# Optimization experiments

Hardware: AMD Instinct MI355X
Metric: run time of the kernel (lower is better)

## Reference

```python
import jax, jax.numpy as jnp
import numpy as np

NUM_ENTITIES = 100000
NUM_RELATIONS = 500
DIM = 256
NUM_TRIANGLES = 300000
NUM_TETRAS = 150000
ET_EDGES = 900000   # ~3 entities per triangle
TT_EDGES = 600000   # ~4 triangles per tetra
ENT_TET_EDGES = 600000
BATCH = 8192


def _mean_aggregate(src_idx, dst_idx, src, num_dst):
    """Scatter-mean of src[src_idx] into num_dst buckets keyed by dst_idx."""
    agg = jax.ops.segment_sum(src[src_idx], dst_idx, num_segments=num_dst)
    cnt = jax.ops.segment_sum(jnp.ones_like(dst_idx, dtype=src.dtype), dst_idx,
                              num_segments=num_dst)
    return agg / jnp.maximum(cnt, 1.0)[:, None]


def setup_inputs() -> dict:
    key = jax.random.key(0)
    ks = jax.random.split(key, 16)
    s = 1.0 / np.sqrt(DIM)
    E = jax.random.normal(ks[0], (NUM_ENTITIES, DIM), jnp.float32) * s
    R = jax.random.normal(ks[1], (NUM_RELATIONS, DIM), jnp.float32) * s
    lin2_w = jax.random.normal(ks[2], (DIM, DIM), jnp.float32) * s
    lin2_b = jnp.zeros((DIM,), jnp.float32)
    lin3_w = jax.random.normal(ks[3], (DIM, DIM), jnp.float32) * s
    lin3_b = jnp.zeros((DIM,), jnp.float32)
    t2e_w = jax.random.normal(ks[4], (DIM, DIM), jnp.float32) * s
    t2e_b = jnp.zeros((DIM,), jnp.float32)
    fusion_alpha = jnp.zeros((2,), jnp.float32)
    gamma = jnp.array([12.0], jnp.float32)
    # bipartite edge lists: row 0 = src indices, row 1 = dst indices
    et = jnp.stack([
        jax.random.randint(ks[5], (ET_EDGES,), 0, NUM_ENTITIES),
        jax.random.randint(ks[6], (ET_EDGES,), 0, NUM_TRIANGLES)], axis=0)
    tt = jnp.stack([
        jax.random.randint(ks[7], (TT_EDGES,), 0, NUM_TRIANGLES),
        jax.random.randint(ks[8], (TT_EDGES,), 0, NUM_TETRAS)], axis=0)
    # entity_tetra_index: row 0 = entity, row 1 = tetra (flipped inside model)
    etet = jnp.stack([
        jax.random.randint(ks[9], (ENT_TET_EDGES,), 0, NUM_ENTITIES),
        jax.random.randint(ks[10], (ENT_TET_EDGES,), 0, NUM_TETRAS)], axis=0)
    triples = jnp.stack([
        jax.random.randint(ks[11], (BATCH,), 0, NUM_ENTITIES),
        jax.random.randint(ks[12], (BATCH,), 0, NUM_RELATIONS),
        jax.random.randint(ks[13], (BATCH,), 0, NUM_ENTITIES)], axis=1)
    return {"E": E, "R": R, "lin2_w": lin2_w, "lin2_b": lin2_b,
            "lin3_w": lin3_w, "lin3_b": lin3_b, "t2e_w": t2e_w, "t2e_b": t2e_b,
            "fusion_alpha": fusion_alpha, "gamma": gamma,
            "entity_triangle_index": et, "triangle_tetra_index": tt,
            "entity_tetra_index": etet, "triples": triples,
            "num_triangles": NUM_TRIANGLES, "num_tetras": NUM_TETRAS}


def reference(E, R, lin2_w, lin2_b, lin3_w, lin3_b, t2e_w, t2e_b,
              fusion_alpha, gamma, entity_triangle_index, triangle_tetra_index,
              entity_tetra_index, triples, num_triangles, num_tetras):
    # gnn2: entity -> triangle (scatter-mean + Linear + ReLU)
    tri_agg = _mean_aggregate(entity_triangle_index[0], entity_triangle_index[1],
                              E, num_triangles)                      # [T, d]
    tri_emb = jax.nn.relu(tri_agg @ lin2_w.T + lin2_b)
    # gnn3: triangle -> tetra
    tet_agg = _mean_aggregate(triangle_tetra_index[0], triangle_tetra_index[1],
                              tri_emb, num_tetras)                   # [K, d]
    tet_emb = jax.nn.relu(tet_agg @ lin3_w.T + lin3_b)
    tet_proj = tet_emb @ t2e_w.T + t2e_b                             # [K, d]
    # tetra -> entity (edge index flipped: src=tetra, dst=entity)
    v_topo = _mean_aggregate(entity_tetra_index[1], entity_tetra_index[0],
                             tet_proj, E.shape[0])                   # [N, d]
    # learned fusion
    w = jax.nn.softmax(fusion_alpha)
    V = w[0] * E + w[1] * v_topo
    # TransE scoring: gamma - ||V[h] + R[r] - V[t]||
    h, r, t = triples[:, 0], triples[:, 1], triples[:, 2]
    diff = V[h] + R[r] - V[t]
    return gamma[0] - jnp.sqrt(jnp.sum(diff * diff, axis=-1))
```

## Files before the change

### kernel.cpp

```cpp
#include <hip/hip_runtime.h>
#include <hip/hip_bf16.h>
#include <math.h>

#define DIM 256
#define SBS 256
#define SIT 16
#define NT   300000
#define NTET 150000

typedef __attribute__((ext_vector_type(8))) short          bf16x8;
typedef __attribute__((ext_vector_type(8))) unsigned short u16x8;
typedef __attribute__((ext_vector_type(4))) float          f32x4;

__device__ inline float b2f(unsigned short u) {
    union { unsigned int i; float f; } c; c.i = ((unsigned int)u) << 16; return c.f;
}
__device__ inline unsigned short f2b(float f) {
    __hip_bfloat16 h = __float2bfloat16(f);
    return *reinterpret_cast<unsigned short*>(&h);
}
__device__ inline short f2bs(float f) { return (short)f2b(f); }
__device__ inline bool bmget(const unsigned* bm, int i) {
    return (bm[i >> 5] >> (i & 31)) & 1u;
}
__device__ inline void gll16(const void* g, void* l) {
    __builtin_amdgcn_global_load_lds(
        (const __attribute__((address_space(1))) unsigned int*)g,
        (__attribute__((address_space(3))) unsigned int*)l, 16, 0, 0);
}

__global__ __launch_bounds__(256) void k_cast3(
    const float* __restrict__ w2, const float* __restrict__ w3,
    const float* __restrict__ wt, unsigned short* __restrict__ out)
{
    int i = (blockIdx.x * 256 + threadIdx.x) * 4;
    const float* src; int l;
    if (i < 65536)       { src = w2; l = i; }
    else if (i < 131072) { src = w3; l = i - 65536; }
    else                 { src = wt; l = i - 131072; }
    float4 v = *(const float4*)(src + l);
    ushort4 o; o.x = f2b(v.x); o.y = f2b(v.y); o.z = f2b(v.z); o.w = f2b(v.w);
    *(ushort4*)(out + i) = o;
}

__global__ __launch_bounds__(256) void k_mark(
    const int* __restrict__ trip, unsigned* __restrict__ bm, int B)
{
    int i = blockIdx.x * 256 + threadIdx.x;
    if (i < 2 * B) {
        int ent = trip[(i >> 1) * 3 + ((i & 1) ? 2 : 0)];
        atomicOr(&bm[ent >> 5], 1u << (ent & 31));
    }
}

__global__ __launch_bounds__(256) void k_markf(
    const int* __restrict__ mi, const int* __restrict__ ci,
    const unsigned* __restrict__ bmIn, unsigned* __restrict__ bmOut, int n)
{
    int e = blockIdx.x * 256 + threadIdx.x;
    if (e < n && bmget(bmIn, ci[e])) {
        int m = mi[e];
        unsigned msk = 1u << (m & 31);
        if (!(bmOut[m >> 5] & msk)) atomicOr(&bmOut[m >> 5], msk);
    }
}

__global__ __launch_bounds__(256) void k_bits(
    const unsigned* __restrict__ bm, int* __restrict__ out, int n)
{
    int i = blockIdx.x * 256 + threadIdx.x;
    if (i < n) out[i] = (bm[i >> 5] >> (i & 31)) & 1u;
}

__global__ __launch_bounds__(256) void k_count_all(
    const int* __restrict__ et, const int* __restrict__ tt, const int* __restrict__ etet,
    const unsigned* __restrict__ bmTri, const unsigned* __restrict__ bmTet,
    const unsigned* __restrict__ bmEnt, int* __restrict__ cnt,
    int ET, int TT, int ETET)
{
    int e = blockIdx.x * 256 + threadIdx.x;
    if (e < ET) {
        int d = et[ET + e];
        if (bmget(bmTri, d)) atomicAdd(&cnt[d], 1);
    } else if (e < ET + TT) {
        int i = e - ET;
        int d = tt[TT + i];
        if (bmget(bmTet, d)) atomicAdd(&cnt[NT + d], 1);
    } else if (e < ET + TT + ETET) {
        int i = e - ET - TT;
        int d = etet[i];
        if (bmget(bmEnt, d)) atomicAdd(&cnt[NT + NTET + d], 1);
    }
}

__global__ __launch_bounds__(SBS) void k_scan_block(
    const int* __restrict__ cnt, int* __restrict__ rowOff,
    int* __restrict__ blockSums, int n)
{
    __shared__ int lds[SBS];
    const int t = threadIdx.x;
    const int tbase = blockIdx.x * SBS * SIT + t * SIT;
    int v[SIT]; int tsum = 0;
    #pragma unroll
    for (int i = 0; i < SIT; ++i) {
        int idx = tbase + i;
        v[i] = (idx < n) ? cnt[idx] : 0;
        tsum += v[i];
    }
    lds[t] = tsum;
    __syncthreads();
    #pragma unroll
    for (int off = 1; off < SBS; off <<= 1) {
        int y = (t >= off) ? lds[t - off] : 0;
        __syncthreads();
        lds[t] += y;
        __syncthreads();
    }
    int incl = lds[t];
    int run = incl - tsum;
    #pragma unroll
    for (int i = 0; i < SIT; ++i) {
        int idx = tbase + i;
        if (idx < n) rowOff[idx] = run;
        run += v[i];
    }
    if (t == SBS - 1) blockSums[blockIdx.x] = incl;
}

__global__ __launch_bounds__(SBS) void k_scan_sums(int* __restrict__ bs, int nb)
{
    __shared__ int lds[SBS];
    const int t = threadIdx.x;
    int v = (t < nb) ? bs[t] : 0;
    lds[t] = v;
    __syncthreads();
    #pragma unroll
    for (int off = 1; off < SBS; off <<= 1) {
        int y = (t >= off) ? lds[t - off] : 0;
        __syncthreads();
        lds[t] += y;
        __syncthreads();
    }
    if (t < nb) {
        bs[t] = lds[t] - v;
        if (t == nb - 1) bs[nb] = lds[t];
    }
}

__global__ __launch_bounds__(256) void k_scan_add(
    int* __restrict__ rowOff, int* __restrict__ cursor,
    const int* __restrict__ bs, int n, int nb, int ncur)
{
    int i = blockIdx.x * 256 + threadIdx.x;
    if (i < n) {
        int v = rowOff[i] + bs[i / (SBS * SIT)];
        rowOff[i] = v;
        if (i < ncur) cursor[i] = v;
    }
    if (i == 0) rowOff[n] = bs[nb];
}

__global__ __launch_bounds__(256) void k_place_all(
    const int* __restrict__ et, const int* __restrict__ tt, const int* __restrict__ etet,
    const unsigned* __restrict__ bmTri, const unsigned* __restrict__ bmTet,
    const unsigned* __restrict__ bmEnt, int* __restrict__ cursor,
    int* __restrict__ sorted, int ET, int TT, int ETET)
{
    int e = blockIdx.x * 256 + threadIdx.x;
    if (e < ET) {
        int d = et[ET + e];
        if (bmget(bmTri, d)) sorted[atomicAdd(&cursor[d], 1)] = et[e];
    } else if (e < ET + TT) {
        int i = e - ET;
        int d = tt[TT + i];
        if (bmget(bmTet, d)) sorted[atomicAdd(&cursor[NT + d], 1)] = tt[i];
    } else if (e < ET + TT + ETET) {
        int i = e - ET - TT;
        int d = etet[i];
        if (bmget(bmEnt, d)) sorted[atomicAdd(&cursor[NT + NTET + d], 1)] = etet[ETET + i];
    }
}

template<int EPI>
__global__ __launch_bounds__(256) void k_gather(
    const unsigned short* __restrict__ src, const int* __restrict__ sorted,
    const int* __restrict__ rowOff, const float* __restrict__ bias,
    const float* __restrict__ E, const float* __restrict__ alpha,
    const unsigned* __restrict__ bm, const int* __restrict__ cmpOff,
    void* __restrict__ out, int ndst)
{
    const int g    = (blockIdx.x * 256 + threadIdx.x) >> 6;
    const int lane = threadIdx.x & 63;
    const int half = lane >> 5;
    const int hl   = lane & 31;
    const int dA   = g * 4 + half * 2;
    const int dB   = dA + 1;
    const bool needA = (dA < ndst) && bmget(bm, dA);
    const bool needB = (dB < ndst) && bmget(bm, dB);
    if (!__any(needA || needB)) return;
    const int cmpBase = (EPI >= 1) ? cmpOff[0] : 0;
    int e0A = 0, e1A = 0, e0B = 0, e1B = 0;
    if (needA) { e0A = rowOff[dA]; e1A = rowOff[dA + 1]; }
    if (needB) { e0B = rowOff[dB]; e1B = rowOff[dB + 1]; }
    const int lenA = e1A - e0A, lenB = e1B - e0B;
    const int mx = lenA > lenB ? lenA : lenB;
    float accA[8] = {0.f,0.f,0.f,0.f,0.f,0.f,0.f,0.f};
    float accB[8] = {0.f,0.f,0.f,0.f,0.f,0.f,0.f,0.f};
    for (int p = 0; p < mx; p += 4) {
        u16x8 uA[4], uB[4]; float gA[4], gB[4];
        #pragma unroll
        for (int j = 0; j < 4; ++j) {
            int eA = e0A + p + j;
            bool vA = eA < e1A;
            int sA = sorted[vA ? eA : 0];
            if (EPI == 2) sA = cmpOff[sA] - cmpBase;
            sA = vA ? sA : 0;
            uA[j] = *(const u16x8*)(src + (size_t)sA * DIM + hl * 8);
            gA[j] = vA ? 1.0f : 0.0f;
            int eB = e0B + p + j;
            bool vB = eB < e1B;
            int sB = sorted[vB ? eB : 0];
            if (EPI == 2) sB = cmpOff[sB] - cmpBase;
            sB = vB ? sB : 0;
            uB[j] = *(const u16x8*)(src + (size_t)sB * DIM + hl * 8);
            gB[j] = vB ? 1.0f : 0.0f;
        }
        #pragma unroll
        for (int j = 0; j < 4; ++j)
            #pragma unroll
            for (int k = 0; k < 8; ++k) {
                accA[k] += gA[j] * b2f(uA[j][k]);
                accB[k] += gB[j] * b2f(uB[j][k]);
            }
    }
    const float invA = 1.0f / fmaxf((float)lenA, 1.0f);
    const float invB = 1.0f / fmaxf((float)lenB, 1.0f);
    #pragma unroll
    for (int k = 0; k < 8; ++k) { accA[k] *= invA; accB[k] *= invB; }
    if (EPI == 0) {
        float4 bl = *(const float4*)(bias + hl * 8);
        float4 bh = *(const float4*)(bias + hl * 8 + 4);
        float bb[8] = {bl.x, bl.y, bl.z, bl.w, bh.x, bh.y, bh.z, bh.w};
        if (needA) {
            u16x8 o;
            #pragma unroll
            for (int k = 0; k < 8; ++k) o[k] = f2b(fmaxf(accA[k] + bb[k], 0.f));
            *(u16x8*)((unsigned short*)out + (size_t)dA * DIM + hl * 8) = o;
        }
        if (needB) {
            u16x8 o;
            #pragma unroll
            for (int k = 0; k < 8; ++k) o[k] = f2b(fmaxf(accB[k] + bb[k], 0.f));
            *(u16x8*)((unsigned short*)out + (size_t)dB * DIM + hl * 8) = o;
        }
    } else if (EPI == 1) {
        if (needA) {
            int cd = cmpOff[dA] - cmpBase;
            u16x8 o;
            #pragma unroll
            for (int k = 0; k < 8; ++k) o[k] = f2b(accA[k]);
            *(u16x8*)((unsigned short*)out + (size_t)cd * DIM + hl * 8) = o;
        }
        if (needB) {
            int cd = cmpOff[dB] - cmpBase;
            u16x8 o;
            #pragma unroll
            for (int k = 0; k < 8; ++k) o[k] = f2b(accB[k]);
            *(u16x8*)((unsigned short*)out + (size_t)cd * DIM + hl * 8) = o;
        }
    } else {
        float a0 = alpha[0], a1v = alpha[1];
        float mxv = fmaxf(a0, a1v);
        float x0 = expf(a0 - mxv), x1 = expf(a1v - mxv);
        float w0 = x0 / (x0 + x1), w1 = x1 / (x0 + x1);
        if (needA) {
            const float* er = E + (size_t)dA * DIM + hl * 8;
            float4 el = *(const float4*)er;
            float4 eh = *(const float4*)(er + 4);
            float4 o0, o1;
            o0.x = w0 * el.x + w1 * accA[0]; o0.y = w0 * el.y + w1 * accA[1];
            o0.z = w0 * el.z + w1 * accA[2]; o0.w = w0 * el.w + w1 * accA[3];
            o1.x = w0 * eh.x + w1 * accA[4]; o1.y = w0 * eh.y + w1 * accA[5];
            o1.z = w0 * eh.z + w1 * accA[6]; o1.w = w0 * eh.w + w1 * accA[7];
            float* orow = (float*)out + (size_t)dA * DIM + hl * 8;
            *(float4*)orow = o0;
            *(float4*)(orow + 4) = o1;
        }
        if (needB) {
            const float* er = E + (size_t)dB * DIM + hl * 8;
            float4 el = *(const float4*)er;
            float4 eh = *(const float4*)(er + 4);
            float4 o0, o1;
            o0.x = w0 * el.x + w1 * accB[0]; o0.y = w0 * el.y + w1 * accB[1];
            o0.z = w0 * el.z + w1 * accB[2]; o0.w = w0 * el.w + w1 * accB[3];
            o1.x = w0 * eh.x + w1 * accB[4]; o1.y = w0 * eh.y + w1 * accB[5];
            o1.z = w0 * eh.z + w1 * accB[6]; o1.w = w0 * eh.w + w1 * accB[7];
            float* orow = (float*)out + (size_t)dB * DIM + hl * 8;
            *(float4*)orow = o0;
            *(float4*)(orow + 4) = o1;
        }
    }
}

template<int MR, bool AF32, bool RELU, bool BIAS, bool DYNM>
__global__ __launch_bounds__(256) void k_gemm_mfma(
    const void* __restrict__ Ap, const unsigned short* __restrict__ Wb,
    const float* __restrict__ bias, unsigned short* __restrict__ Cp,
    int Ms, const int* __restrict__ cmpOff)
{
    int M = Ms;
    if (DYNM) M = cmpOff[NTET] - cmpOff[0];
    const int m0 = blockIdx.x * MR;
    if (m0 >= M) return;
    constexpr int ABYTES = MR * 64 * (AF32 ? 4 : 2);
    __shared__ __align__(16) char smem[ABYTES + 16384];
    char* AsB = smem;
    char* WsB = smem + ABYTES;
    const int tid  = threadIdx.x;
    const int n0   = blockIdx.y * 128;
    const int wid  = tid >> 6, lane = tid & 63;
    const int wr   = wid >> 1, wc = wid & 1;
    const int fr   = lane & 15;
    const int fc   = lane >> 4;
    constexpr int MFR = MR / 32;

    f32x4 acc[MFR][4] = {};
    for (int k0 = 0; k0 < DIM; k0 += 64) {
        __syncthreads();
        if (AF32) {
            #pragma unroll
            for (int it = 0; it < MR / 16; ++it) {
                int q = it * 256 + tid;
                int r = q >> 4, s = q & 15;
                int gm = m0 + r; if (gm >= M) gm = M - 1;
                int sp = s ^ (r & 15);
                gll16((const float*)Ap + (size_t)gm * DIM + k0 + sp * 4,
                      AsB + (size_t)q * 16);
            }
        } else {
            #pragma unroll
            for (int it = 0; it < MR / 32; ++it) {
                int q = it * 256 + tid;
                int r = q >> 3, s = q & 7;
                int gm = m0 + r; if (gm >= M) gm = M - 1;
                int sp = s ^ (r & 7);
                gll16((const unsigned short*)Ap + (size_t)gm * DIM + k0 + sp * 8,
                      AsB + (size_t)q * 16);
            }
        }
        #pragma unroll
        for (int it = 0; it < 4; ++it) {
            int q = it * 256 + tid;
            int r = q >> 3, s = q & 7;
            int sp = s ^ (r & 7);
            gll16(Wb + (size_t)(n0 + r) * DIM + k0 + sp * 8,
                  WsB + (size_t)q * 16);
        }
        __syncthreads();
        #pragma unroll
        for (int kk = 0; kk < 2; ++kk) {
            bf16x8 aF[MFR], bF[4];
            #pragma unroll
            for (int i = 0; i < 4; ++i) {
                int wn = wc * 64 + i * 16 + fr;
                int pw = kk * 4 + fc;
                bF[i] = *(const bf16x8*)(WsB + wn * 128 + ((pw ^ (wn & 7)) * 16));
            }
            #pragma unroll
            for (int i = 0; i < MFR; ++i) {
                int ar = wr * (MFR * 16) + i * 16 + fr;
                if (AF32) {
                    int p0 = kk * 8 + fc * 2;
                    const char* rb = AsB + ar * 256;
                    float4 lo = *(const float4*)(rb + ((p0       ^ (ar & 15)) * 16));
                    float4 hi = *(const float4*)(rb + (((p0 + 1) ^ (ar & 15)) * 16));
                    bf16x8 a;
                    a[0] = f2bs(lo.x); a[1] = f2bs(lo.y); a[2] = f2bs(lo.z); a[3] = f2bs(lo.w);
                    a[4] = f2bs(hi.x); a[5] = f2bs(hi.y); a[6] = f2bs(hi.z); a[7] = f2bs(hi.w);
                    aF[i] = a;
                } else {
                    int p = kk * 4 + fc;
                    aF[i] = *(const bf16x8*)(AsB + ar * 128 + ((p ^ (ar & 7)) * 16));
                }
            }
            #pragma unroll
            for (int i = 0; i < MFR; ++i)
                #pragma unroll
                for (int j = 0; j < 4; ++j)
                    acc[i][j] = __builtin_amdgcn_mfma_f32_16x16x32_bf16(
                        aF[i], bF[j], acc[i][j], 0, 0, 0);
        }
    }
    const int cnb   = n0 + wc * 64 + fr;
    const int rbase = m0 + wr * (MFR * 16) + fc * 4;
    #pragma unroll
    for (int j = 0; j < 4; ++j) {
        float bv = BIAS ? bias[cnb + j * 16] : 0.0f;
        #pragma unroll
        for (int i = 0; i < MFR; ++i) {
            #pragma unroll
            for (int q = 0; q < 4; ++q) {
                int m = rbase + i * 16 + q;
                if (m < M) {
                    float v = acc[i][j][q] + bv;
                    if (RELU) v = fmaxf(v, 0.f);
                    Cp[(size_t)m * DIM + cnb + j * 16] = f2b(v);
                }
            }
        }
    }
}

__global__ __launch_bounds__(256) void k_score(
    const float* __restrict__ V, const float* __restrict__ R,
    const int* __restrict__ triples, const float* __restrict__ gamma,
    float* __restrict__ out, int B)
{
    int t    = (blockIdx.x * 256 + threadIdx.x) >> 6;
    int lane = threadIdx.x & 63;
    if (t >= B) return;
    int h  = triples[t * 3 + 0];
    int r  = triples[t * 3 + 1];
    int tl = triples[t * 3 + 2];
    float4 vh = *(const float4*)(V + (size_t)h  * DIM + lane * 4);
    float4 vr = *(const float4*)(R + (size_t)r  * DIM + lane * 4);
    float4 vt = *(const float4*)(V + (size_t)tl * DIM + lane * 4);
    float dx = vh.x + vr.x - vt.x;
    float dy = vh.y + vr.y - vt.y;
    float dz = vh.z + vr.z - vt.z;
    float dw = vh.w + vr.w - vt.w;
    float s = dx * dx + dy * dy + dz * dz + dw * dw;
    #pragma unroll
    for (int off = 32; off > 0; off >>= 1) s += __shfl_xor(s, off);
    if (lane == 0) out[t] = gamma[0] - sqrtf(s);
}

extern "C" void kernel_launch(void* const* d_in, const int* in_sizes, int n_in,
                              void* d_out, int out_size, void* d_ws, size_t ws_size,
                              hipStream_t stream)
{
    const float* E      = (const float*)d_in[0];
    const float* R      = (const float*)d_in[1];
    const float* lin2_w = (const float*)d_in[2];
    const float* lin2_b = (const float*)d_in[3];
    const float* lin3_w = (const float*)d_in[4];
    const float* lin3_b = (const float*)d_in[5];
    const float* t2e_w  = (const float*)d_in[6];
    const float* t2e_b  = (const float*)d_in[7];
    const float* alpha  = (const float*)d_in[8];
    const float* gamma  = (const float*)d_in[9];
    const int*   et     = (const int*)d_in[10];
    const int*   tt     = (const int*)d_in[11];
    const int*   etet   = (const int*)d_in[12];
    const int*   trip   = (const int*)d_in[13];

    const int NE    = in_sizes[0] / DIM;
    const int ET    = in_sizes[10] / 2;
    const int TT    = in_sizes[11] / 2;
    const int ETET  = in_sizes[12] / 2;
    const int B     = in_sizes[13] / 3;
    const int NTOT  = NT + NTET + NE;
    const int NTOT2 = NTOT + NTET;
    const int ETOT  = ET + TT + ETET;

    char* ws = (char*)d_ws;
    const size_t P1  = (size_t)NE * DIM * 4;
    const size_t IDX = P1 + (size_t)NT * DIM * 2;
    unsigned short* EW      = (unsigned short*)ws;
    unsigned short* tetAgg  = (unsigned short*)ws;
    float*          V       = (float*)ws;
    unsigned short* triEmb  = (unsigned short*)(ws + P1);
    unsigned short* tetEmb  = (unsigned short*)(ws + P1);
    unsigned short* tetProj = (unsigned short*)(ws + P1) + (size_t)NTET * DIM;
    size_t off = IDX;
    int* sortedAll = (int*)(ws + off); off += (size_t)ETOT * 4;
    int* rowOffAll = (int*)(ws + off); off += ((size_t)(NTOT2 + 1) * 4 + 15) & ~15ull;
    int* cursorAll = (int*)(ws + off); off += (size_t)NTOT * 4;
    int* blockSums = (int*)(ws + off); off += 1040;
    unsigned short* Wb = (unsigned short*)(ws + off); off += 3 * 131072;
    char* zbase = ws + off;
    int*      cntAll = (int*)(ws + off);      off += (size_t)NTOT2 * 4;
    unsigned* bmEnt  = (unsigned*)(ws + off); off += ((size_t)(NE   + 31) / 32) * 4;
    unsigned* bmTet  = (unsigned*)(ws + off); off += ((size_t)(NTET + 31) / 32) * 4;
    unsigned* bmTri  = (unsigned*)(ws + off); off += ((size_t)(NT   + 31) / 32) * 4;
    size_t zsize = (size_t)(ws + off - zbase);
    if (ws_size < off) return;

    unsigned short* W2b = Wb;
    unsigned short* W3b = Wb + 65536;
    unsigned short* Wtb = Wb + 131072;
    int* cmpOff = rowOffAll + NTOT;

    hipMemsetAsync(zbase, 0, zsize, stream);
    k_cast3<<<192, 256, 0, stream>>>(lin2_w, lin3_w, t2e_w, Wb);
    dim3 gE((NE + 63) / 64, 2);
    k_gemm_mfma<64, true, false, false, false><<<gE, 256, 0, stream>>>(
        E, W2b, nullptr, EW, NE, nullptr);

    k_mark<<<(2 * B + 255) / 256, 256, 0, stream>>>(trip, bmEnt, B);
    k_markf<<<(ETET + 255) / 256, 256, 0, stream>>>(etet + ETET, etet, bmEnt, bmTet, ETET);
    k_markf<<<(TT + 255) / 256, 256, 0, stream>>>(tt, tt + TT, bmTet, bmTri, TT);
    k_bits<<<(NTET + 255) / 256, 256, 0, stream>>>(bmTet, cntAll + NTOT, NTET);

    k_count_all<<<(ETOT + 255) / 256, 256, 0, stream>>>(
        et, tt, etet, bmTri, bmTet, bmEnt, cntAll, ET, TT, ETET);
    int nb = (NTOT2 + SBS * SIT - 1) / (SBS * SIT);
    k_scan_block<<<nb, SBS, 0, stream>>>(cntAll, rowOffAll, blockSums, NTOT2);
    k_scan_sums<<<1, SBS, 0, stream>>>(blockSums, nb);
    k_scan_add<<<(NTOT2 + 255) / 256, 256, 0, stream>>>(rowOffAll, cursorAll,
                                                        blockSums, NTOT2, nb, NTOT);
    k_place_all<<<(ETOT + 255) / 256, 256, 0, stream>>>(
        et, tt, etet, bmTri, bmTet, bmEnt, cursorAll, sortedAll, ET, TT, ETET);

    k_gather<0><<<(NT + 15) / 16, 256, 0, stream>>>(EW, sortedAll, rowOffAll, lin2_b,
                                                    nullptr, nullptr, bmTri, cmpOff,
                                                    triEmb, NT);

    k_gather<1><<<(NTET + 15) / 16, 256, 0, stream>>>(triEmb, sortedAll, rowOffAll + NT,
                                                      nullptr, nullptr, nullptr, bmTet,
                                                      cmpOff, tetAgg, NTET);
    dim3 gT((NTET + 127) / 128, 2);
    k_gemm_mfma<128, false, true, true, true><<<gT, 256, 0, stream>>>(
        tetAgg, W3b, lin3_b, tetEmb, NTET, cmpOff);
    k_gemm_mfma<128, false, false, true, true><<<gT, 256, 0, stream>>>(
        tetEmb, Wtb, t2e_b, tetProj, NTET, cmpOff);

    k_gather<2><<<(NE + 15) / 16, 256, 0, stream>>>(tetProj, sortedAll,
                                                    rowOffAll + NT + NTET, nullptr,
                                                    E, alpha, bmEnt, cmpOff, V, NE);

    k_score<<<(B + 3) / 4, 256, 0, stream>>>(V, R, trip, gamma, (float*)d_out, B);
}
```

Measured before the change: 427.9 us.

## Merge small setup kernels, fold block-sum scan into scan_add, split gather loop

Fuses the weight cast with triple marking, folds the tetra bit-to-count step into the count kernel, and removes the separate block-sum scan by having each scan_add block reduce the block sums it needs. It also adds a predicate-free main loop in the gather for the shared full-length prefix of paired rows, and raises the entity GEMM tile from 64 to 128 rows. The goal is fewer launches and less per-edge masking, at the cost of redundant block-sum reductions in every scan_add block.

Result: slower. 446.5 us (+4.3%).

```diff
diff --git a/kernel.cpp b/kernel.cpp
--- a/kernel.cpp
+++ b/kernel.cpp
@@ -29,27 +29,27 @@
         (__attribute__((address_space(3))) unsigned int*)l, 16, 0, 0);
 }
 
-__global__ __launch_bounds__(256) void k_cast3(
+__global__ __launch_bounds__(256) void k_init(
     const float* __restrict__ w2, const float* __restrict__ w3,
-    const float* __restrict__ wt, unsigned short* __restrict__ out)
-{
-    int i = (blockIdx.x * 256 + threadIdx.x) * 4;
-    const float* src; int l;
-    if (i < 65536)       { src = w2; l = i; }
-    else if (i < 131072) { src = w3; l = i - 65536; }
-    else                 { src = wt; l = i - 131072; }
-    float4 v = *(const float4*)(src + l);
-    ushort4 o; o.x = f2b(v.x); o.y = f2b(v.y); o.z = f2b(v.z); o.w = f2b(v.w);
-    *(ushort4*)(out + i) = o;
-}
-
-__global__ __launch_bounds__(256) void k_mark(
+    const float* __restrict__ wt, unsigned short* __restrict__ out,
     const int* __restrict__ trip, unsigned* __restrict__ bm, int B)
 {
-    int i = blockIdx.x * 256 + threadIdx.x;
-    if (i < 2 * B) {
-        int ent = trip[(i >> 1) * 3 + ((i & 1) ? 2 : 0)];
-        atomicOr(&bm[ent >> 5], 1u << (ent & 31));
+    int b = blockIdx.x;
+    if (b < 192) {
+        int i = (b * 256 + threadIdx.x) * 4;
+        const float* src; int l;
+        if (i < 65536)       { src = w2; l = i; }
+        else if (i < 131072) { src = w3; l = i - 65536; }
+        else                 { src = wt; l = i - 131072; }
+        float4 v = *(const float4*)(src + l);
+        ushort4 o; o.x = f2b(v.x); o.y = f2b(v.y); o.z = f2b(v.z); o.w = f2b(v.w);
+        *(ushort4*)(out + i) = o;
+    } else {
+        int i = (b - 192) * 256 + threadIdx.x;
+        if (i < 2 * B) {
+            int ent = trip[(i >> 1) * 3 + ((i & 1) ? 2 : 0)];
+            atomicOr(&bm[ent >> 5], 1u << (ent & 31));
+        }
     }
 }
 
@@ -65,18 +65,11 @@
     }
 }
 
-__global__ __launch_bounds__(256) void k_bits(
-    const unsigned* __restrict__ bm, int* __restrict__ out, int n)
-{
-    int i = blockIdx.x * 256 + threadIdx.x;
-    if (i < n) out[i] = (bm[i >> 5] >> (i & 31)) & 1u;
-}
-
 __global__ __launch_bounds__(256) void k_count_all(
     const int* __restrict__ et, const int* __restrict__ tt, const int* __restrict__ etet,
     const unsigned* __restrict__ bmTri, const unsigned* __restrict__ bmTet,
     const unsigned* __restrict__ bmEnt, int* __restrict__ cnt,
-    int ET, int TT, int ETET)
+    int ET, int TT, int ETET, int NTOT)
 {
     int e = blockIdx.x * 256 + threadIdx.x;
     if (e < ET) {
@@ -90,6 +83,9 @@
         int i = e - ET - TT;
         int d = etet[i];
         if (bmget(bmEnt, d)) atomicAdd(&cnt[NT + NTET + d], 1);
+    } else if (e < ET + TT + ETET + NTET) {
+        int i = e - ET - TT - ETET;
+        cnt[NTOT + i] = bmget(bmTet, i) ? 1 : 0;
     }
 }
 
@@ -127,37 +123,35 @@
     if (t == SBS - 1) blockSums[blockIdx.x] = incl;
 }
 
-__global__ __launch_bounds__(SBS) void k_scan_sums(int* __restrict__ bs, int nb)
-{
-    __shared__ int lds[SBS];
-    const int t = threadIdx.x;
-    int v = (t < nb) ? bs[t] : 0;
-    lds[t] = v;
-    __syncthreads();
-    #pragma unroll
-    for (int off = 1; off < SBS; off <<= 1) {
-        int y = (t >= off) ? lds[t - off] : 0;
-        __syncthreads();
-        lds[t] += y;
-        __syncthreads();
-    }
-    if (t < nb) {
-        bs[t] = lds[t] - v;
-        if (t == nb - 1) bs[nb] = lds[t];
-    }
-}
-
 __global__ __launch_bounds__(256) void k_scan_add(
     int* __restrict__ rowOff, int* __restrict__ cursor,
     const int* __restrict__ bs, int n, int nb, int ncur)
 {
-    int i = blockIdx.x * 256 + threadIdx.x;
+    __shared__ int red[2][4];
+    __shared__ int basev, totv;
+    const int t = threadIdx.x;
+    const int seg = blockIdx.x / 16;
+    int vs = (t < seg) ? bs[t] : 0;
+    int va = (t < nb)  ? bs[t] : 0;
+    #pragma unroll
+    for (int off = 32; off > 0; off >>= 1) {
+        vs += __shfl_down(vs, off);
+        va += __shfl_down(va, off);
+    }
+    if ((t & 63) == 0) { red[0][t >> 6] = vs; red[1][t >> 6] = va; }
+    __syncthreads();
+    if (t == 0) {
+        basev = red[0][0] + red[0][1] + red[0][2] + red[0][3];
+        totv  = red[1][0] + red[1][1] + red[1][2] + red[1][3];
+    }
+    __syncthreads();
+    int i = blockIdx.x * 256 + t;
     if (i < n) {
-        int v = rowOff[i] + bs[i / (SBS * SIT)];
+        int v = rowOff[i] + basev;
         rowOff[i] = v;
         if (i < ncur) cursor[i] = v;
     }
-    if (i == 0) rowOff[n] = bs[nb];
+    if (i == 0) rowOff[n] = totv;
 }
 
 __global__ __launch_bounds__(256) void k_place_all(
@@ -203,10 +197,31 @@
     if (needA) { e0A = rowOff[dA]; e1A = rowOff[dA + 1]; }
     if (needB) { e0B = rowOff[dB]; e1B = rowOff[dB + 1]; }
     const int lenA = e1A - e0A, lenB = e1B - e0B;
+    const int minl = (lenA < lenB ? lenA : lenB) & ~3;
     const int mx = lenA > lenB ? lenA : lenB;
     float accA[8] = {0.f,0.f,0.f,0.f,0.f,0.f,0.f,0.f};
     float accB[8] = {0.f,0.f,0.f,0.f,0.f,0.f,0.f,0.f};
-    for (int p = 0; p < mx; p += 4) {
+    int p = 0;
+    for (; p < minl; p += 4) {
+        u16x8 uA[4], uB[4];
+        #pragma unroll
+        for (int j = 0; j < 4; ++j) {
+            int sA = sorted[e0A + p + j];
+            if (EPI == 2) sA = cmpOff[sA] - cmpBase;
+            uA[j] = *(const u16x8*)(src + (size_t)sA * DIM + hl * 8);
+            int sB = sorted[e0B + p + j];
+            if (EPI == 2) sB = cmpOff[sB] - cmpBase;
+            uB[j] = *(const u16x8*)(src + (size_t)sB * DIM + hl * 8);
+        }
+        #pragma unroll
+        for (int j = 0; j < 4; ++j)
+            #pragma unroll
+            for (int k = 0; k < 8; ++k) {
+                accA[k] += b2f(uA[j][k]);
+                accB[k] += b2f(uB[j][k]);
+            }
+    }
+    for (; p < mx; p += 4) {
         u16x8 uA[4], uB[4]; float gA[4], gB[4];
         #pragma unroll
         for (int j = 0; j < 4; ++j) {
@@ -492,21 +507,19 @@
     int* cmpOff = rowOffAll + NTOT;
 
     hipMemsetAsync(zbase, 0, zsize, stream);
-    k_cast3<<<192, 256, 0, stream>>>(lin2_w, lin3_w, t2e_w, Wb);
-    dim3 gE((NE + 63) / 64, 2);
-    k_gemm_mfma<64, true, false, false, false><<<gE, 256, 0, stream>>>(
+    k_init<<<192 + (2 * B + 255) / 256, 256, 0, stream>>>(
+        lin2_w, lin3_w, t2e_w, Wb, trip, bmEnt, B);
+    dim3 gE((NE + 127) / 128, 2);
+    k_gemm_mfma<128, true, false, false, false><<<gE, 256, 0, stream>>>(
         E, W2b, nullptr, EW, NE, nullptr);
 
-    k_mark<<<(2 * B + 255) / 256, 256, 0, stream>>>(trip, bmEnt, B);
     k_markf<<<(ETET + 255) / 256, 256, 0, stream>>>(etet + ETET, etet, bmEnt, bmTet, ETET);
     k_markf<<<(TT + 255) / 256, 256, 0, stream>>>(tt, tt + TT, bmTet, bmTri, TT);
-    k_bits<<<(NTET + 255) / 256, 256, 0, stream>>>(bmTet, cntAll + NTOT, NTET);
-
-    k_count_all<<<(ETOT + 255) / 256, 256, 0, stream>>>(
-        et, tt, etet, bmTri, bmTet, bmEnt, cntAll, ET, TT, ETET);
+
+    k_count_all<<<(ETOT + NTET + 255) / 256, 256, 0, stream>>>(
+        et, tt, etet, bmTri, bmTet, bmEnt, cntAll, ET, TT, ETET, NTOT);
     int nb = (NTOT2 + SBS * SIT - 1) / (SBS * SIT);
     k_scan_block<<<nb, SBS, 0, stream>>>(cntAll, rowOffAll, blockSums, NTOT2);
-    k_scan_sums<<<1, SBS, 0, stream>>>(blockSums, nb);
     k_scan_add<<<(NTOT2 + 255) / 256, 256, 0, stream>>>(rowOffAll, cursorAll,
                                                         blockSums, NTOT2, nb, NTOT);
     k_place_all<<<(ETOT + 255) / 256, 256, 0, stream>>>(
```
